# Optimization experiments

Hardware: AMD Instinct MI355X
Metric: run time of the kernel (lower is better)

## Reference

```python
import jax, jax.numpy as jnp
import numpy as np

EPS = 1e-8


def _conv1(x, w):
    # x: [C,H,W], w: [O,C,k,k] -> [O,H,W] (SAME padding, stride 1)
    return jax.lax.conv_general_dilated(
        x[None], w, window_strides=(1, 1), padding='SAME',
        dimension_numbers=('NCHW', 'OIHW', 'NCHW'))[0]


def setup_inputs() -> dict:
    key = jax.random.key(0)
    k1, k2, k3, k4 = jax.random.split(key, 4)
    B, C, O, K, S, H, W = 8, 512, 512, 3, 512, 64, 64
    inp = jax.random.normal(k1, (B, C, H, W), dtype=jnp.float32)
    style = jax.random.normal(k2, (B, S), dtype=jnp.float32)
    weight = jax.random.normal(k3, (1, O, C, K, K), dtype=jnp.float32)  # conv weight
    mod_weight = jax.random.normal(k4, (C, S), dtype=jnp.float32)      # EqualLinear weight
    mod_bias = jnp.ones((C,), dtype=jnp.float32)                        # bias filled with 1.0
    return {"input": inp, "style": style, "weight": weight,
            "mod_weight": mod_weight, "mod_bias": mod_bias}


def reference(input, style, weight, mod_weight, mod_bias) -> jnp.ndarray:
    B, C, H, W = input.shape
    _, O, _, K, _ = weight.shape
    fan_in = C * K * K
    scale = 1.0 / np.sqrt(fan_in)
    lin_scale = 1.0 / np.sqrt(mod_weight.shape[1])

    # EqualLinear modulation: [B, C]
    s = style @ (mod_weight * lin_scale).T + mod_bias

    # Modulate + demodulate per-sample weights: [B, O, C, K, K]
    w = scale * weight * s[:, None, :, None, None]
    demod = jax.lax.rsqrt(jnp.sum(w * w, axis=(2, 3, 4)) + EPS)  # [B, O]
    w = w * demod[:, :, None, None, None]

    # Grouped conv with groups=B == per-sample conv, vmapped over batch
    out = jax.vmap(_conv1)(input, w)  # [B, O, H, W]
    return out
```

## Files before the change

kernel.cpp:

```cpp
#include <hip/hip_runtime.h>

typedef unsigned short u16;
typedef __bf16 bf16_t;
typedef bf16_t bf16x8 __attribute__((ext_vector_type(8)));
typedef float floatx4 __attribute__((ext_vector_type(4)));

static constexpr float kScale = 0.014731391274719741f;
static constexpr float kScale2 = 2.1701388888888894e-4f;
static constexpr float kLinScale = 0.044194173824159216f;

__device__ __forceinline__ u16 f2bf(float f) {
  unsigned u = __float_as_uint(f);
  u += 0x7FFFu + ((u >> 16) & 1u);
  return (u16)(u >> 16);
}

#define GLD16(g, l)                                                        \
  __builtin_amdgcn_global_load_lds(                                        \
      (const __attribute__((address_space(1))) unsigned int*)(g),          \
      (__attribute__((address_space(3))) unsigned int*)(l), 16, 0, 0)

__global__ __launch_bounds__(256) void k_prep1(const float* __restrict__ style,
                                               const float* __restrict__ modw,
                                               const float* __restrict__ modb,
                                               const float* __restrict__ weight,
                                               float* __restrict__ s_buf,
                                               float* __restrict__ ssq) {
  int tid = threadIdx.x;
  if (blockIdx.x < 1024) {
    int lane = tid & 63, wv = tid >> 6;
    int idx = blockIdx.x * 4 + wv;
    int b = idx >> 9, c = idx & 511;
    const float* st = style + b * 512;
    const float* mw = modw + (size_t)c * 512;
    float s = 0.f;
#pragma unroll
    for (int i = 0; i < 8; ++i) s += st[lane + i * 64] * mw[lane + i * 64];
#pragma unroll
    for (int off = 32; off; off >>= 1) s += __shfl_xor(s, off);
    if (lane == 0) s_buf[idx] = s * kLinScale + modb[c];
  } else {
    int e = (blockIdx.x - 1024) * 256 + tid;
    const float* wp = weight + (size_t)e * 9;
    float ss = 0.f;
#pragma unroll
    for (int t = 0; t < 9; ++t) ss += wp[t] * wp[t];
    ssq[e] = ss;
  }
}

__global__ __launch_bounds__(256) void k_demod2(const float* __restrict__ ssq,
                                                const float* __restrict__ s_buf,
                                                float* __restrict__ demod_buf) {
  int tid = threadIdx.x, lane = tid & 63, wv = tid >> 6;
  int idx = blockIdx.x * 4 + wv;
  int b = idx >> 9, o = idx & 511;
  const float* sq = ssq + (size_t)o * 512;
  const float* srow = s_buf + b * 512;
  float ss = 0.f;
#pragma unroll
  for (int i = 0; i < 8; ++i) {
    float s = srow[lane + i * 64];
    ss += sq[lane + i * 64] * s * s;
  }
#pragma unroll
  for (int off = 32; off; off >>= 1) ss += __shfl_xor(ss, off);
  if (lane == 0) demod_buf[idx] = rsqrtf(ss * kScale2 + 1e-8f);
}

__global__ __launch_bounds__(256) void k_transpose(const float* __restrict__ in,
                                                   const float* __restrict__ s_buf,
                                                   unsigned* __restrict__ in_t32) {
  __shared__ u16 tile[64 * 65];
  int tid = threadIdx.x;
  int c0 = blockIdx.x * 64, y = blockIdx.y, b = blockIdx.z;
  const float* src = in + ((size_t)(b * 512 + c0) * 4096) + y * 64;
  const float* srow = s_buf + b * 512 + c0;
#pragma unroll
  for (int it = 0; it < 16; ++it) {
    int idx = it * 256 + tid;
    int cl = idx >> 6, x = idx & 63;
    tile[cl * 65 + x] = f2bf(src[(size_t)cl * 4096 + x] * srow[cl]);
  }
  __syncthreads();
  unsigned* dst = in_t32 + ((size_t)(b * 64 + y) * 64) * 256 + (c0 >> 1);
#pragma unroll
  for (int it = 0; it < 8; ++it) {
    int flat = it * 256 + tid;
    int cl2 = flat & 31, x = flat >> 5;
    unsigned lo = tile[(2 * cl2) * 65 + x];
    unsigned hi = tile[(2 * cl2 + 1) * 65 + x];
    dst[(size_t)x * 256 + cl2] = lo | (hi << 16);
  }
}

__global__ __launch_bounds__(256) void k_wfrag(const float* __restrict__ weight,
                                               unsigned* __restrict__ wt32) {
  __shared__ u16 tiles[9][512];
  int tid = threadIdx.x;
  int ct = blockIdx.x, ot = blockIdx.y;
  int o0 = ot * 16, c0 = ct * 32;
#pragma unroll
  for (int i = 0; i < 18; ++i) {
    int flat = i * 256 + tid;
    int t9 = flat / 9;
    int tap = flat - t9 * 9;
    int o_l = t9 >> 5, c_l = t9 & 31;
    float w = weight[((size_t)(o0 + o_l) * 512 + c0 + c_l) * 9 + tap];
    int pos = ((o_l + ((c_l >> 3) << 4)) << 3) + (c_l & 7);
    tiles[tap][pos] = f2bf(w * kScale);
  }
  __syncthreads();
  const unsigned* tl = (const unsigned*)tiles;
#pragma unroll
  for (int tap = 0; tap < 9; ++tap)
    wt32[(size_t)((tap * 16 + ct) * 32 + ot) * 256 + tid] = tl[tap * 256 + tid];
}

__global__ __launch_bounds__(256, 2) void k_conv(const u16* __restrict__ in_t,
                                                 const u16* __restrict__ w_t,
                                                 const float* __restrict__ demod_buf,
                                                 float* __restrict__ out) {
  __shared__ char smem[32768];
  const int tid = threadIdx.x;
  const int lane = tid & 63;
  const int wv = tid >> 6;
  const int wm = wv >> 1, wn = wv & 1;
  const int quad = lane >> 4, m16 = lane & 15;
  const int lin = blockIdx.x + 32 * blockIdx.y + 128 * blockIdx.z;
  const int b = lin & 7;
  const int r_ = lin >> 3;
  const int nt = r_ & 31;
  const int mt = r_ >> 5;
  const int y0 = nt * 2;

  floatx4 acc[4][4];
#pragma unroll
  for (int i = 0; i < 4; ++i)
#pragma unroll
    for (int j = 0; j < 4; ++j) acc[i][j] = (floatx4){0.f, 0.f, 0.f, 0.f};

  const u16* abase = w_t + mt * 4096 + wm * 2048 + lane * 8;

#define STAGE_B(ct_, Bbuf)                                                   \
  {                                                                          \
    const int c0s = (ct_)*32;                                                \
    _Pragma("unroll") for (int r = 0; r < 4; ++r) {                          \
      const int ci = r * 256 + tid;                                          \
      const int s = ci >> 2, qi = ci & 3;                                    \
      const int x = s & 63;                                                  \
      const int y = y0 - 1 + r;                                              \
      const int qd = qi ^ (x & 3);                                           \
      char* lbase = (Bbuf) + (r * 4 + wv) * 1024;                            \
      if ((unsigned)y < 64u) {                                               \
        const u16* g =                                                       \
            in_t + (((size_t)(b * 64 + y) * 64 + x) * 512 + c0s + qd * 8);   \
        GLD16(g, lbase);                                                     \
      } else {                                                               \
        *(uint4*)((Bbuf) + ci * 16) = make_uint4(0u, 0u, 0u, 0u);            \
      }                                                                      \
    }                                                                        \
  }

#define LOAD_A(tap_, ct_, dst)                                               \
  {                                                                          \
    const u16* ap_ = abase + ((size_t)((tap_)*16 + (ct_)) << 14);            \
    _Pragma("unroll") for (int ms = 0; ms < 4; ++ms)                         \
      (dst)[ms] = *(const bf16x8*)(ap_ + ms * 512);                          \
  }

  STAGE_B(0, smem);
  bf16x8 aR0[4], aR1[4], aR2[4];
  LOAD_A(0, 0, aR0);
  LOAD_A(1, 0, aR1);
  __syncthreads();

  int cur = 0;
  for (int ct = 0; ct < 16; ++ct) {
    char* Bs = smem + cur * 16384;
    char* Bn = smem + (cur ^ 1) * 16384;
    if (ct < 15) STAGE_B(ct + 1, Bn);
#pragma unroll
    for (int t = 0; t < 9; ++t) {
      const int dy = t / 3, dx = t % 3;
      const int tp = (t + 2 <= 8) ? t + 2 : t - 7;
      const int ctp = (t + 2 <= 8) ? ct : ((ct + 1) & 15);
      if (t % 3 == 0) {
        LOAD_A(tp, ctp, aR2);
      } else if (t % 3 == 1) {
        LOAD_A(tp, ctp, aR0);
      } else {
        LOAD_A(tp, ctp, aR1);
      }
      const bf16x8* afc = (t % 3 == 0) ? aR0 : (t % 3 == 1) ? aR1 : aR2;
      __builtin_amdgcn_s_setprio(1);
#pragma unroll
      for (int ns = 0; ns < 4; ++ns) {
        const int nl = wn * 64 + ns * 16 + m16;
        const int ly = nl >> 6, lx = nl & 63;
        const int sx = lx + dx - 1;
        bf16x8 bv;
        if ((unsigned)sx < 64u) {
          const int s = (ly + dy) * 64 + sx;
          bv = *(const bf16x8*)(Bs + s * 64 + ((quad ^ (sx & 3)) << 4));
        } else {
#pragma unroll
          for (int j = 0; j < 8; ++j) bv[j] = (bf16_t)0.f;
        }
#pragma unroll
        for (int ms = 0; ms < 4; ++ms)
          acc[ms][ns] = __builtin_amdgcn_mfma_f32_16x16x32_bf16(
              afc[ms], bv, acc[ms][ns], 0, 0, 0);
      }
      __builtin_amdgcn_s_setprio(0);
    }
    __syncthreads();
    cur ^= 1;
  }

#undef STAGE_B
#undef LOAD_A

  const int ob = mt * 128 + wm * 64;
  const int nb = nt * 128 + wn * 64;
#pragma unroll
  for (int ms = 0; ms < 4; ++ms)
#pragma unroll
    for (int ns = 0; ns < 4; ++ns) {
      const int n = nb + ns * 16 + m16;
#pragma unroll
      for (int r = 0; r < 4; ++r) {
        const int o = ob + ms * 16 + quad * 4 + r;
        float dm = demod_buf[b * 512 + o];
        out[((size_t)(b * 512 + o) << 12) + n] = acc[ms][ns][r] * dm;
      }
    }
}

extern "C" void kernel_launch(void* const* d_in, const int* in_sizes, int n_in,
                              void* d_out, int out_size, void* d_ws, size_t ws_size,
                              hipStream_t stream) {
  const float* input = (const float*)d_in[0];
  const float* style = (const float*)d_in[1];
  const float* weight = (const float*)d_in[2];
  const float* modw = (const float*)d_in[3];
  const float* modb = (const float*)d_in[4];
  float* out = (float*)d_out;
  char* ws = (char*)d_ws;
  float* s_buf = (float*)ws;
  float* demod_buf = (float*)(ws + 16384);
  float* ssq = (float*)(ws + 32768);
  u16* in_t = (u16*)(ws + 32768 + 1048576);
  u16* w_t = (u16*)(ws + 32768 + 1048576 + 33554432);

  k_prep1<<<dim3(2048), dim3(256), 0, stream>>>(style, modw, modb, weight, s_buf, ssq);
  k_demod2<<<dim3(1024), dim3(256), 0, stream>>>(ssq, s_buf, demod_buf);
  k_transpose<<<dim3(8, 64, 8), dim3(256), 0, stream>>>(input, s_buf, (unsigned*)in_t);
  k_wfrag<<<dim3(16, 32), dim3(256), 0, stream>>>(weight, (unsigned*)w_t);
  k_conv<<<dim3(32, 4, 8), dim3(256), 0, stream>>>(in_t, w_t, demod_buf, out);
}
```

Baseline: 256.1 us.

## Triple-buffer input tiles and prefetch B fragments one tap ahead in registers

Expands LDS from two to three input-channel stages so global-to-LDS loads run two chunks ahead. B operand fragments are now read from LDS one tap in advance into rotating registers, overlapping LDS reads with MFMA work. The LDS swizzle changes from x&3 to (x>>1)&3 to alter the bank-conflict pattern. The cost is more LDS per block (48KB, which may limit two blocks per CU) and more VGPRs, which risks lower occupancy or spills under launch_bounds(256,2).

Result: no change. 255.2 us (-0.3%).

```diff
diff --git a/kernel.cpp b/kernel.cpp
--- a/kernel.cpp
+++ b/kernel.cpp
@@ -121,7 +121,7 @@
                                                  const u16* __restrict__ w_t,
                                                  const float* __restrict__ demod_buf,
                                                  float* __restrict__ out) {
-  __shared__ char smem[32768];
+  __shared__ char smem[49152];
   const int tid = threadIdx.x;
   const int lane = tid & 63;
   const int wv = tid >> 6;
@@ -150,7 +150,7 @@
       const int s = ci >> 2, qi = ci & 3;                                    \
       const int x = s & 63;                                                  \
       const int y = y0 - 1 + r;                                              \
-      const int qd = qi ^ (x & 3);                                           \
+      const int qd = qi ^ ((x >> 1) & 3);                                    \
       char* lbase = (Bbuf) + (r * 4 + wv) * 1024;                            \
       if ((unsigned)y < 64u) {                                               \
         const u16* g =                                                       \
@@ -169,57 +169,82 @@
       (dst)[ms] = *(const bf16x8*)(ap_ + ms * 512);                          \
   }
 
+#define LOAD_BV(dst, Bsrc, t_)                                               \
+  {                                                                          \
+    const int dy_ = (t_) / 3, dx_ = (t_) % 3;                                \
+    _Pragma("unroll") for (int ns = 0; ns < 4; ++ns) {                       \
+      const int nl = wn * 64 + ns * 16 + m16;                                \
+      const int ly = nl >> 6, lx = nl & 63;                                  \
+      const int sx = lx + dx_ - 1;                                           \
+      if ((unsigned)sx < 64u) {                                              \
+        const int s = (ly + dy_) * 64 + sx;                                  \
+        (dst)[ns] = *(const bf16x8*)((Bsrc) + s * 64 +                       \
+                                     ((quad ^ ((sx >> 1) & 3)) << 4));       \
+      } else {                                                               \
+        _Pragma("unroll") for (int j = 0; j < 8; ++j) (dst)[ns][j] =         \
+            (bf16_t)0.f;                                                     \
+      }                                                                      \
+    }                                                                        \
+  }
+
+#define T_BODY(t_, BCUR, BNXT, ACUR, ANXT)                                   \
+  {                                                                          \
+    const int tp_ = ((t_) + 2 <= 8) ? (t_) + 2 : (t_)-7;                     \
+    const int ctp_ = ((t_) + 2 <= 8) ? ct : ((ct + 1) & 15);                 \
+    LOAD_A(tp_, ctp_, ANXT);                                                 \
+    if ((t_) < 8) {                                                          \
+      LOAD_BV(BNXT, Bs, (t_) + 1);                                           \
+    } else {                                                                 \
+      LOAD_BV(BNXT, Bn, 0);      \
+    }                                                                        \
+    __builtin_amdgcn_s_setprio(1);                                           \
+    _Pragma("unroll") for (int ns = 0; ns < 4; ++ns) {                       \
+      _Pragma("unroll") for (int ms = 0; ms < 4; ++ms)                       \
+        acc[ms][ns] = __builtin_amdgcn_mfma_f32_16x16x32_bf16(               \
+            (ACUR)[ms], (BCUR)[ns], acc[ms][ns], 0, 0, 0);                   \
+    }                                                                        \
+    __builtin_amdgcn_s_setprio(0);                                           \
+  }
+
   STAGE_B(0, smem);
+  STAGE_B(1, smem + 16384);
   bf16x8 aR0[4], aR1[4], aR2[4];
   LOAD_A(0, 0, aR0);
   LOAD_A(1, 0, aR1);
   __syncthreads();
 
-  int cur = 0;
+  bf16x8 bv0[4], bv1[4], bv2[4];
+  {
+    char* Bs = smem;
+    LOAD_BV(bv0, Bs, 0);
+  }
+
+  char* Bs = smem;
+  char* Bn = smem + 16384;
+  char* Bs2 = smem + 32768;
   for (int ct = 0; ct < 16; ++ct) {
-    char* Bs = smem + cur * 16384;
-    char* Bn = smem + (cur ^ 1) * 16384;
-    if (ct < 15) STAGE_B(ct + 1, Bn);
+    if (ct < 14) STAGE_B(ct + 2, Bs2);
 #pragma unroll
     for (int t = 0; t < 9; ++t) {
-      const int dy = t / 3, dx = t % 3;
-      const int tp = (t + 2 <= 8) ? t + 2 : t - 7;
-      const int ctp = (t + 2 <= 8) ? ct : ((ct + 1) & 15);
       if (t % 3 == 0) {
-        LOAD_A(tp, ctp, aR2);
+        T_BODY(t, bv0, bv1, aR0, aR2);
       } else if (t % 3 == 1) {
-        LOAD_A(tp, ctp, aR0);
+        T_BODY(t, bv1, bv2, aR1, aR0);
       } else {
-        LOAD_A(tp, ctp, aR1);
+        T_BODY(t, bv2, bv0, aR2, aR1);
       }
-      const bf16x8* afc = (t % 3 == 0) ? aR0 : (t % 3 == 1) ? aR1 : aR2;
-      __builtin_amdgcn_s_setprio(1);
-#pragma unroll
-      for (int ns = 0; ns < 4; ++ns) {
-        const int nl = wn * 64 + ns * 16 + m16;
-        const int ly = nl >> 6, lx = nl & 63;
-        const int sx = lx + dx - 1;
-        bf16x8 bv;
-        if ((unsigned)sx < 64u) {
-          const int s = (ly + dy) * 64 + sx;
-          bv = *(const bf16x8*)(Bs + s * 64 + ((quad ^ (sx & 3)) << 4));
-        } else {
-#pragma unroll
-          for (int j = 0; j < 8; ++j) bv[j] = (bf16_t)0.f;
-        }
-#pragma unroll
-        for (int ms = 0; ms < 4; ++ms)
-          acc[ms][ns] = __builtin_amdgcn_mfma_f32_16x16x32_bf16(
-              afc[ms], bv, acc[ms][ns], 0, 0, 0);
-      }
-      __builtin_amdgcn_s_setprio(0);
     }
     __syncthreads();
-    cur ^= 1;
+    char* tmp = Bs;
+    Bs = Bn;
+    Bn = Bs2;
+    Bs2 = tmp;
   }
 
 #undef STAGE_B
 #undef LOAD_A
+#undef LOAD_BV
+#undef T_BODY
 
   const int ob = mt * 128 + wm * 64;
   const int nb = nt * 128 + wn * 64;
```
